# Optimization experiments

Measured on AMD Instinct MI355X. Metric: run time of the kernel, lower is better.

## Reference

```python
import jax, jax.numpy as jnp
import numpy as np

N_NODES = 100000
N_EDGES = 1600000
IN_C, HID, OUT_C = 128, 128, 64
LN_EPS = 1e-5


def _glorot(key, shape):
    fan_in = shape[-1]
    return jax.random.normal(key, shape, dtype=jnp.float32) / jnp.sqrt(jnp.float32(fan_in))


def setup_inputs() -> dict:
    key = jax.random.key(0)
    ks = jax.random.split(key, 16)
    x = jax.random.normal(ks[0], (N_NODES, IN_C), dtype=jnp.float32)
    edge_index = jax.random.randint(ks[1], (2, N_EDGES), 0, N_NODES, dtype=jnp.int64)
    inp = {"x": x, "edge_index": edge_index}
    dims = [(IN_C, HID), (HID, HID), (HID, OUT_C)]
    for i, (din, dout) in enumerate(dims):
        inp[f"Wl{i}"] = _glorot(ks[2 + 3 * i], (dout, din))   # neighbor-aggregate weight
        inp[f"Wr{i}"] = _glorot(ks[3 + 3 * i], (dout, din))   # root/self weight
        inp[f"b{i}"] = jnp.zeros((dout,), dtype=jnp.float32)
    for i, d in enumerate([HID, HID]):
        inp[f"g{i}"] = jnp.ones((d,), dtype=jnp.float32)      # LayerNorm gamma
        inp[f"be{i}"] = jnp.zeros((d,), dtype=jnp.float32)    # LayerNorm beta
    return inp


def sage_conv(x, src, dst, Wl, Wr, b):
    # mean aggregation of source features at destination nodes
    msg = x[src]                                                    # [E, F]
    agg = jax.ops.segment_sum(msg, dst, num_segments=N_NODES)      # [N, F]
    deg = jax.ops.segment_sum(jnp.ones((src.shape[0],), x.dtype), dst, num_segments=N_NODES)
    agg = agg / jnp.maximum(deg, 1.0)[:, None]
    return agg @ Wl.T + x @ Wr.T + b


def layer_norm(x, gamma, beta):
    mu = jnp.mean(x, axis=-1, keepdims=True)
    var = jnp.mean(jnp.square(x - mu), axis=-1, keepdims=True)
    return (x - mu) * jax.lax.rsqrt(var + LN_EPS) * gamma + beta


def reference(x, edge_index, Wl0, Wr0, b0, g0, be0, Wl1, Wr1, b1, g1, be1, Wl2, Wr2, b2):
    src, dst = edge_index[0], edge_index[1]
    h = layer_norm(jax.nn.relu(sage_conv(x, src, dst, Wl0, Wr0, b0)), g0, be0)
    h = layer_norm(jax.nn.relu(sage_conv(h, src, dst, Wl1, Wr1, b1)), g1, be1)
    return sage_conv(h, src, dst, Wl2, Wr2, b2)
```

## Files before the change

### kernel.cpp

```cpp
#include <hip/hip_runtime.h>


typedef __bf16 bf16x8 __attribute__((ext_vector_type(8)));
typedef __bf16 bf16x4 __attribute__((ext_vector_type(4)));
typedef float  f32x4  __attribute__((ext_vector_type(4)));

#define PB_SHIFT 9
#define PB_NB    256
#define PB_EPT   8
#define PB_BLOCK 256
#define PB_CHUNK (PB_BLOCK * PB_EPT)

__global__ __launch_bounds__(PB_BLOCK) void coarse_hist(
    const int* __restrict__ dst, int* __restrict__ bhist, int E) {
    __shared__ int h[PB_NB];
    const int t = threadIdx.x;
    h[t] = 0;
    __syncthreads();
    const int e0 = blockIdx.x * PB_CHUNK + t;
#pragma unroll
    for (int i = 0; i < PB_EPT; ++i) {
        int e = e0 + i * PB_BLOCK;
        if (e < E) atomicAdd(&h[dst[e] >> PB_SHIFT], 1);
    }
    __syncthreads();
    if (h[t]) atomicAdd(&bhist[t], h[t]);
}

__global__ __launch_bounds__(PB_NB) void coarse_scan(
    const int* __restrict__ bhist, int* __restrict__ bbase, int* __restrict__ bcur) {
    __shared__ int sm[PB_NB];
    const int t = threadIdx.x;
    int v = bhist[t];
    sm[t] = v;
    __syncthreads();
    for (int off = 1; off < PB_NB; off <<= 1) {
        int add = (t >= off) ? sm[t - off] : 0;
        __syncthreads();
        sm[t] += add;
        __syncthreads();
    }
    int excl = sm[t] - v;
    bbase[t] = excl;
    bcur[t] = excl;
}

__global__ __launch_bounds__(PB_BLOCK) void part_scatter(
    const int* __restrict__ src, const int* __restrict__ dst,
    int* __restrict__ bcursor, int2* __restrict__ part, int E) {
    __shared__ int hist[PB_NB];
    __shared__ int base[PB_NB];
    const int t = threadIdx.x;
    hist[t] = 0;
    __syncthreads();
    const int e0 = blockIdx.x * PB_CHUNK + t;
    int my_s[PB_EPT], my_d[PB_EPT], my_r[PB_EPT];
#pragma unroll
    for (int i = 0; i < PB_EPT; ++i) {
        int e = e0 + i * PB_BLOCK;
        if (e < E) {
            my_s[i] = src[e];
            my_d[i] = dst[e];
            my_r[i] = atomicAdd(&hist[my_d[i] >> PB_SHIFT], 1);
        }
    }
    __syncthreads();
    {
        int c = hist[t];
        base[t] = c ? atomicAdd(&bcursor[t], c) : 0;
    }
    __syncthreads();
#pragma unroll
    for (int i = 0; i < PB_EPT; ++i) {
        int e = e0 + i * PB_BLOCK;
        if (e < E) {
            int b = my_d[i] >> PB_SHIFT;
            part[base[b] + my_r[i]] = make_int2(my_s[i], my_d[i]);
        }
    }
}

__global__ __launch_bounds__(256) void bucket_build(
    const int2* __restrict__ part, const int* __restrict__ bbase,
    int* __restrict__ offs, int* __restrict__ ssrc, int N, int E) {
    __shared__ int h[512];
    __shared__ int s[512];
    __shared__ int cur[512];
    const int b = blockIdx.x;
    const int t = threadIdx.x;
    const int beg = bbase[b];
    const int end = (b == PB_NB - 1) ? E : bbase[b + 1];

    h[t] = 0; h[t + 256] = 0;
    __syncthreads();
    for (int e = beg + t; e < end; e += 256)
        atomicAdd(&h[part[e].y & 511], 1);
    __syncthreads();
    s[t] = h[t]; s[t + 256] = h[t + 256];
    __syncthreads();
    for (int off = 1; off < 512; off <<= 1) {
        int a0 = (t >= off) ? s[t - off] : 0;
        int i1 = t + 256;
        int a1 = (i1 >= off) ? s[i1 - off] : 0;
        __syncthreads();
        s[t] += a0; s[i1] += a1;
        __syncthreads();
    }
#pragma unroll
    for (int k = 0; k < 2; ++k) {
        int i = t + k * 256;
        int excl = s[i] - h[i];
        cur[i] = excl;
        int node = (b << PB_SHIFT) + i;
        if (node < N) offs[node] = beg + excl;
    }
    if (b == 0 && t == 0) offs[N] = E;
    __syncthreads();
    for (int e = beg + t; e < end; e += 256) {
        int2 sd = part[e];
        int p = atomicAdd(&cur[sd.y & 511], 1);
        ssrc[beg + p] = sd.x;
    }
}

template <typename AT, typename ZT>
__global__ __launch_bounds__(256) void gemm_mfma(
    const AT* __restrict__ A,
    const float* __restrict__ Wl,
    const float* __restrict__ Wr,
    const float* __restrict__ bias,
    __bf16* __restrict__ ybuf,
    ZT*     __restrict__ zbuf,
    int M, int dout) {
    __shared__ __bf16 Asm[64 * 136];
    __shared__ __bf16 Bsm[64 * 136];

    const int t = threadIdx.x;
    const int rowBase = blockIdx.x * 64;
    const int by = blockIdx.y;
    const int nyHalf = dout >> 6;
    const bool isZ = by >= nyHalf;
    const float* W = isZ ? Wr : Wl;
    const int colLocal = (by - (isZ ? nyHalf : 0)) * 64;

    if constexpr (sizeof(AT) == 4) {
#pragma unroll
        for (int i = 0; i < 8; ++i) {
            int idx = t + 256 * i;
            int r = idx >> 5;
            int c4 = idx & 31;
            int grow = rowBase + r;
            if (grow >= M) grow = M - 1;
            float4 v = *(const float4*)((const float*)A + (size_t)grow * 128 + c4 * 4);
            bf16x4 o;
            o[0] = (__bf16)v.x; o[1] = (__bf16)v.y; o[2] = (__bf16)v.z; o[3] = (__bf16)v.w;
            *(bf16x4*)(Asm + r * 136 + c4 * 4) = o;
        }
    } else {
#pragma unroll
        for (int i = 0; i < 4; ++i) {
            int idx = t + 256 * i;
            int r = idx >> 4;
            int c8 = idx & 15;
            int grow = rowBase + r;
            if (grow >= M) grow = M - 1;
            bf16x8 v = *(const bf16x8*)((const __bf16*)A + (size_t)grow * 128 + c8 * 8);
            *(bf16x8*)(Asm + r * 136 + c8 * 8) = v;
        }
    }
#pragma unroll
    for (int i = 0; i < 8; ++i) {
        int idx = t + 256 * i;
        int r = idx >> 5;
        int c4 = idx & 31;
        float4 v = *(const float4*)(W + (size_t)(colLocal + r) * 128 + c4 * 4);
        bf16x4 o;
        o[0] = (__bf16)v.x; o[1] = (__bf16)v.y; o[2] = (__bf16)v.z; o[3] = (__bf16)v.w;
        *(bf16x4*)(Bsm + r * 136 + c4 * 4) = o;
    }
    __syncthreads();

    const int lane = t & 63;
    const int wid = t >> 6;
    const int mb = (wid >> 1) * 32;
    const int nb = (wid & 1) * 32;
    const int ln = lane & 15;
    const int qk = lane >> 4;

    f32x4 acc[2][2] = {};
#pragma unroll
    for (int ks = 0; ks < 4; ++ks) {
        const int k0 = ks * 32 + qk * 8;
        bf16x8 a0 = *(const bf16x8*)(Asm + (mb + ln) * 136 + k0);
        bf16x8 a1 = *(const bf16x8*)(Asm + (mb + 16 + ln) * 136 + k0);
        bf16x8 b0 = *(const bf16x8*)(Bsm + (nb + ln) * 136 + k0);
        bf16x8 b1 = *(const bf16x8*)(Bsm + (nb + 16 + ln) * 136 + k0);
        acc[0][0] = __builtin_amdgcn_mfma_f32_16x16x32_bf16(a0, b0, acc[0][0], 0, 0, 0);
        acc[0][1] = __builtin_amdgcn_mfma_f32_16x16x32_bf16(a0, b1, acc[0][1], 0, 0, 0);
        acc[1][0] = __builtin_amdgcn_mfma_f32_16x16x32_bf16(a1, b0, acc[1][0], 0, 0, 0);
        acc[1][1] = __builtin_amdgcn_mfma_f32_16x16x32_bf16(a1, b1, acc[1][1], 0, 0, 0);
    }

#pragma unroll
    for (int i = 0; i < 2; ++i) {
#pragma unroll
        for (int r = 0; r < 4; ++r) {
            int grow = rowBase + mb + i * 16 + qk * 4 + r;
            if (grow >= M) continue;
#pragma unroll
            for (int j = 0; j < 2; ++j) {
                int col = colLocal + nb + j * 16 + ln;
                float v = acc[i][j][r];
                if (isZ) zbuf[(size_t)grow * dout + col] = (ZT)(v + bias[col]);
                else     ybuf[(size_t)grow * dout + col] = (__bf16)v;
            }
        }
    }
}

__global__ __launch_bounds__(256) void agg_ln128(
    const int* __restrict__ offs, const int* __restrict__ ssrc,
    const __bf16* __restrict__ ybuf,
    const __bf16* __restrict__ zbuf,
    const float* __restrict__ gamma, const float* __restrict__ beta,
    __bf16* __restrict__ hout, int nNodes) {
    const int lane = threadIdx.x & 63;
    const int qh = lane >> 4;
    const int li = lane & 15;
    const int node = blockIdx.x * 4 + (threadIdx.x >> 6);
    if (node >= nNodes) return;
    const int beg = offs[node], end = offs[node + 1];

    float acc[8] = {};
    for (int j = beg; j < end; j += 64) {
        int cnt = end - j;
        if (cnt > 64) cnt = 64;
        int sidx = ssrc[j + ((lane < cnt) ? lane : 0)];
        int quads = (cnt + 3) >> 2;
        for (int u = 0; u < quads; ++u) {
            int e = 4 * u + qh;
            int s = __shfl(sidx, (e < cnt) ? e : 0, 64);
            if (e < cnt) {
                bf16x8 v = *(const bf16x8*)(ybuf + (size_t)s * 128 + li * 8);
#pragma unroll
                for (int m = 0; m < 8; ++m) acc[m] += (float)v[m];
            }
        }
    }
#pragma unroll
    for (int m = 0; m < 8; ++m) {
        acc[m] += __shfl_xor(acc[m], 16, 64);
        acc[m] += __shfl_xor(acc[m], 32, 64);
    }
    int degn = end - beg;
    float inv = 1.f / (float)((degn > 1) ? degn : 1);
    bf16x8 zv = *(const bf16x8*)(zbuf + (size_t)node * 128 + li * 8);
    float v[8];
#pragma unroll
    for (int m = 0; m < 8; ++m) v[m] = fmaxf(acc[m] * inv + (float)zv[m], 0.f);

    float s = 0.f;
#pragma unroll
    for (int m = 0; m < 8; ++m) s += v[m];
#pragma unroll
    for (int off = 8; off >= 1; off >>= 1) s += __shfl_xor(s, off, 64);
    float mu = s * (1.f / 128.f);
    float d[8], q = 0.f;
#pragma unroll
    for (int m = 0; m < 8; ++m) { d[m] = v[m] - mu; q += d[m] * d[m]; }
#pragma unroll
    for (int off = 8; off >= 1; off >>= 1) q += __shfl_xor(q, off, 64);
    float rstd = rsqrtf(q * (1.f / 128.f) + 1e-5f);

    if (qh == 0) {
        const float4* g4 = (const float4*)(gamma + li * 8);
        const float4* b4 = (const float4*)(beta + li * 8);
        float4 g0 = g4[0], g1 = g4[1], bb0 = b4[0], bb1 = b4[1];
        bf16x8 o;
        o[0] = (__bf16)(d[0] * rstd * g0.x + bb0.x);
        o[1] = (__bf16)(d[1] * rstd * g0.y + bb0.y);
        o[2] = (__bf16)(d[2] * rstd * g0.z + bb0.z);
        o[3] = (__bf16)(d[3] * rstd * g0.w + bb0.w);
        o[4] = (__bf16)(d[4] * rstd * g1.x + bb1.x);
        o[5] = (__bf16)(d[5] * rstd * g1.y + bb1.y);
        o[6] = (__bf16)(d[6] * rstd * g1.z + bb1.z);
        o[7] = (__bf16)(d[7] * rstd * g1.w + bb1.w);
        *(bf16x8*)(hout + (size_t)node * 128 + li * 8) = o;
    }
}

__global__ __launch_bounds__(256) void agg_out64(
    const int* __restrict__ offs, const int* __restrict__ ssrc,
    const __bf16* __restrict__ ybuf,
    const float* __restrict__ zbuf,
    float* __restrict__ out, int nNodes) {
    const int lane = threadIdx.x & 63;
    const int eh = lane >> 3;
    const int li = lane & 7;
    const int node = blockIdx.x * 4 + (threadIdx.x >> 6);
    if (node >= nNodes) return;
    const int beg = offs[node], end = offs[node + 1];

    float acc[8] = {};
    for (int j = beg; j < end; j += 64) {
        int cnt = end - j;
        if (cnt > 64) cnt = 64;
        int sidx = ssrc[j + ((lane < cnt) ? lane : 0)];
        int octs = (cnt + 7) >> 3;
        for (int u = 0; u < octs; ++u) {
            int e = 8 * u + eh;
            int s = __shfl(sidx, (e < cnt) ? e : 0, 64);
            if (e < cnt) {
                bf16x8 v = *(const bf16x8*)(ybuf + (size_t)s * 64 + li * 8);
#pragma unroll
                for (int m = 0; m < 8; ++m) acc[m] += (float)v[m];
            }
        }
    }
#pragma unroll
    for (int m = 0; m < 8; ++m) {
        acc[m] += __shfl_xor(acc[m], 8, 64);
        acc[m] += __shfl_xor(acc[m], 16, 64);
        acc[m] += __shfl_xor(acc[m], 32, 64);
    }
    if (eh == 0) {
        int degn = end - beg;
        float inv = 1.f / (float)((degn > 1) ? degn : 1);
        const float4* z4 = (const float4*)(zbuf + (size_t)node * 64 + li * 8);
        float4 z0 = z4[0], z1 = z4[1];
        float4 o0, o1;
        o0.x = acc[0] * inv + z0.x;
        o0.y = acc[1] * inv + z0.y;
        o0.z = acc[2] * inv + z0.z;
        o0.w = acc[3] * inv + z0.w;
        o1.x = acc[4] * inv + z1.x;
        o1.y = acc[5] * inv + z1.y;
        o1.z = acc[6] * inv + z1.z;
        o1.w = acc[7] * inv + z1.w;
        float4* op = (float4*)(out + (size_t)node * 64 + li * 8);
        op[0] = o0;
        op[1] = o1;
    }
}

extern "C" void kernel_launch(void* const* d_in, const int* in_sizes, int n_in,
                              void* d_out, int out_size, void* d_ws, size_t ws_size,
                              hipStream_t stream) {
    const float* x   = (const float*)d_in[0];
    const int*   ei  = (const int*)d_in[1];
    const float* Wl0 = (const float*)d_in[2];
    const float* Wr0 = (const float*)d_in[3];
    const float* b0  = (const float*)d_in[4];
    const float* Wl1 = (const float*)d_in[5];
    const float* Wr1 = (const float*)d_in[6];
    const float* b1  = (const float*)d_in[7];
    const float* Wl2 = (const float*)d_in[8];
    const float* Wr2 = (const float*)d_in[9];
    const float* b2  = (const float*)d_in[10];
    const float* g0  = (const float*)d_in[11];
    const float* be0 = (const float*)d_in[12];
    const float* g1  = (const float*)d_in[13];
    const float* be1 = (const float*)d_in[14];

    const int N = in_sizes[0] / 128;
    const int E = in_sizes[1] / 2;
    const int* src = ei;
    const int* dst = ei + E;
    float* out = (float*)d_out;

    char* p = (char*)d_ws;
    auto carve = [&](size_t bytes) {
        void* q = (void*)p;
        p += (bytes + 255) & ~(size_t)255;
        return q;
    };
    int*     offs  = (int*)carve(sizeof(int) * (size_t)(N + 1));
    int*     bhist = (int*)carve(sizeof(int) * (size_t)PB_NB);
    int*     bbase = (int*)carve(sizeof(int) * (size_t)PB_NB);
    int*     bcur  = (int*)carve(sizeof(int) * (size_t)PB_NB);
    int*     ssrc  = (int*)carve(sizeof(int) * (size_t)E);
    int2*    part  = (int2*)carve(sizeof(int2) * (size_t)E);
    __bf16*  h     = (__bf16*)carve(sizeof(__bf16) * (size_t)N * 128);
    __bf16*  ybuf  = (__bf16*)carve(sizeof(__bf16) * (size_t)N * 128);
    void*    zraw  = carve(sizeof(__bf16) * (size_t)N * 128);
    __bf16*  zb    = (__bf16*)zraw;
    float*   zf    = (float*)zraw;

    hipMemsetAsync(bhist, 0, sizeof(int) * PB_NB, stream);
    const int gridE = (E + PB_CHUNK - 1) / PB_CHUNK;
    coarse_hist<<<gridE, PB_BLOCK, 0, stream>>>(dst, bhist, E);
    coarse_scan<<<1, PB_NB, 0, stream>>>(bhist, bbase, bcur);
    part_scatter<<<gridE, PB_BLOCK, 0, stream>>>(src, dst, bcur, part, E);
    bucket_build<<<PB_NB, 256, 0, stream>>>(part, bbase, offs, ssrc, N, E);

    const int gridM = (N + 63) / 64;
    const int gridNode = (N + 3) / 4;

    gemm_mfma<float, __bf16><<<dim3(gridM, 4), 256, 0, stream>>>(x, Wl0, Wr0, b0, ybuf, zb, N, 128);
    agg_ln128<<<gridNode, 256, 0, stream>>>(offs, ssrc, ybuf, zb, g0, be0, h, N);
    gemm_mfma<__bf16, __bf16><<<dim3(gridM, 4), 256, 0, stream>>>(h, Wl1, Wr1, b1, ybuf, zb, N, 128);
    agg_ln128<<<gridNode, 256, 0, stream>>>(offs, ssrc, ybuf, zb, g1, be1, h, N);
    gemm_mfma<__bf16, float><<<dim3(gridM, 2), 256, 0, stream>>>(h, Wl2, Wr2, b2, ybuf, zf, N, 64);
    agg_out64<<<gridNode, 256, 0, stream>>>(offs, ssrc, ybuf, zf, out, N);
}
```

Baseline: 455.4 us.

## Widen GEMM tiles to full output width and prefetch neighbor indices in aggregation

The GEMM kernel is templated on output width so each block computes all output columns for its row tile. This halves the grid and avoids loading and converting the A tile twice per weight. The aggregation kernels replace the chunked shuffle-based index broadcast with direct per-lane index loads, prefetched one iteration ahead, and use bit-shift bf16-to-float conversion. The trade-off is more LDS and accumulator registers per GEMM block and more scalar index loads per lane.

```diff
diff --git a/kernel.cpp b/kernel.cpp
--- a/kernel.cpp
+++ b/kernel.cpp
@@ -123,7 +123,7 @@
     }
 }
 
-template <typename AT, typename ZT>
+template <int DOUT, typename AT, typename ZT>
 __global__ __launch_bounds__(256) void gemm_mfma(
     const AT* __restrict__ A,
     const float* __restrict__ Wl,
@@ -131,17 +131,14 @@
     const float* __restrict__ bias,
     __bf16* __restrict__ ybuf,
     ZT*     __restrict__ zbuf,
-    int M, int dout) {
+    int M) {
     __shared__ __bf16 Asm[64 * 136];
-    __shared__ __bf16 Bsm[64 * 136];
+    __shared__ __bf16 Bsm[DOUT * 136];
 
     const int t = threadIdx.x;
     const int rowBase = blockIdx.x * 64;
-    const int by = blockIdx.y;
-    const int nyHalf = dout >> 6;
-    const bool isZ = by >= nyHalf;
+    const bool isZ = blockIdx.y != 0;
     const float* W = isZ ? Wr : Wl;
-    const int colLocal = (by - (isZ ? nyHalf : 0)) * 64;
 
     if constexpr (sizeof(AT) == 4) {
 #pragma unroll
@@ -168,12 +165,13 @@
             *(bf16x8*)(Asm + r * 136 + c8 * 8) = v;
         }
     }
-#pragma unroll
-    for (int i = 0; i < 8; ++i) {
+    constexpr int BCH = DOUT * 32 / 256;
+#pragma unroll
+    for (int i = 0; i < BCH; ++i) {
         int idx = t + 256 * i;
         int r = idx >> 5;
         int c4 = idx & 31;
-        float4 v = *(const float4*)(W + (size_t)(colLocal + r) * 128 + c4 * 4);
+        float4 v = *(const float4*)(W + (size_t)r * 128 + c4 * 4);
         bf16x4 o;
         o[0] = (__bf16)v.x; o[1] = (__bf16)v.y; o[2] = (__bf16)v.z; o[3] = (__bf16)v.w;
         *(bf16x4*)(Bsm + r * 136 + c4 * 4) = o;
@@ -183,24 +181,33 @@
     const int lane = t & 63;
     const int wid = t >> 6;
     const int mb = (wid >> 1) * 32;
-    const int nb = (wid & 1) * 32;
+    const int nbase = (wid & 1) * (DOUT / 2);
+    constexpr int NJ = DOUT / 32;
     const int ln = lane & 15;
     const int qk = lane >> 4;
 
-    f32x4 acc[2][2] = {};
+    f32x4 acc[2][NJ] = {};
 #pragma unroll
     for (int ks = 0; ks < 4; ++ks) {
         const int k0 = ks * 32 + qk * 8;
         bf16x8 a0 = *(const bf16x8*)(Asm + (mb + ln) * 136 + k0);
         bf16x8 a1 = *(const bf16x8*)(Asm + (mb + 16 + ln) * 136 + k0);
-        bf16x8 b0 = *(const bf16x8*)(Bsm + (nb + ln) * 136 + k0);
-        bf16x8 b1 = *(const bf16x8*)(Bsm + (nb + 16 + ln) * 136 + k0);
-        acc[0][0] = __builtin_amdgcn_mfma_f32_16x16x32_bf16(a0, b0, acc[0][0], 0, 0, 0);
-        acc[0][1] = __builtin_amdgcn_mfma_f32_16x16x32_bf16(a0, b1, acc[0][1], 0, 0, 0);
-        acc[1][0] = __builtin_amdgcn_mfma_f32_16x16x32_bf16(a1, b0, acc[1][0], 0, 0, 0);
-        acc[1][1] = __builtin_amdgcn_mfma_f32_16x16x32_bf16(a1, b1, acc[1][1], 0, 0, 0);
-    }
-
+        bf16x8 b[NJ];
+#pragma unroll
+        for (int j = 0; j < NJ; ++j)
+            b[j] = *(const bf16x8*)(Bsm + (nbase + j * 16 + ln) * 136 + k0);
+#pragma unroll
+        for (int j = 0; j < NJ; ++j) {
+            acc[0][j] = __builtin_amdgcn_mfma_f32_16x16x32_bf16(a0, b[j], acc[0][j], 0, 0, 0);
+            acc[1][j] = __builtin_amdgcn_mfma_f32_16x16x32_bf16(a1, b[j], acc[1][j], 0, 0, 0);
+        }
+    }
+
+    float bcol[NJ];
+    if (isZ) {
+#pragma unroll
+        for (int j = 0; j < NJ; ++j) bcol[j] = bias[nbase + j * 16 + ln];
+    }
 #pragma unroll
     for (int i = 0; i < 2; ++i) {
 #pragma unroll
@@ -208,11 +215,11 @@
             int grow = rowBase + mb + i * 16 + qk * 4 + r;
             if (grow >= M) continue;
 #pragma unroll
-            for (int j = 0; j < 2; ++j) {
-                int col = colLocal + nb + j * 16 + ln;
+            for (int j = 0; j < NJ; ++j) {
+                int col = nbase + j * 16 + ln;
                 float v = acc[i][j][r];
-                if (isZ) zbuf[(size_t)grow * dout + col] = (ZT)(v + bias[col]);
-                else     ybuf[(size_t)grow * dout + col] = (__bf16)v;
+                if (isZ) zbuf[(size_t)grow * DOUT + col] = (ZT)(v + bcol[j]);
+                else     ybuf[(size_t)grow * DOUT + col] = (__bf16)v;
             }
         }
     }
@@ -230,30 +237,35 @@
     const int node = blockIdx.x * 4 + (threadIdx.x >> 6);
     if (node >= nNodes) return;
     const int beg = offs[node], end = offs[node + 1];
+    const int deg = end - beg;
 
     float acc[8] = {};
-    for (int j = beg; j < end; j += 64) {
-        int cnt = end - j;
-        if (cnt > 64) cnt = 64;
-        int sidx = ssrc[j + ((lane < cnt) ? lane : 0)];
-        int quads = (cnt + 3) >> 2;
-        for (int u = 0; u < quads; ++u) {
-            int e = 4 * u + qh;
-            int s = __shfl(sidx, (e < cnt) ? e : 0, 64);
-            if (e < cnt) {
-                bf16x8 v = *(const bf16x8*)(ybuf + (size_t)s * 128 + li * 8);
-#pragma unroll
-                for (int m = 0; m < 8; ++m) acc[m] += (float)v[m];
-            }
-        }
+    const int iters = (deg + 3) >> 2;
+    int e = beg + qh;
+    int idx = 0;
+    if (iters > 0) idx = ssrc[(e < end) ? e : beg];
+    for (int u = 0; u < iters; ++u) {
+        int en = e + 4;
+        int idxN = ssrc[(en < end) ? en : beg];
+        if (e < end) {
+            uint4 uv = *(const uint4*)(ybuf + (size_t)idx * 128 + li * 8);
+            acc[0] += __uint_as_float(uv.x << 16);
+            acc[1] += __uint_as_float(uv.x & 0xffff0000u);
+            acc[2] += __uint_as_float(uv.y << 16);
+            acc[3] += __uint_as_float(uv.y & 0xffff0000u);
+            acc[4] += __uint_as_float(uv.z << 16);
+            acc[5] += __uint_as_float(uv.z & 0xffff0000u);
+            acc[6] += __uint_as_float(uv.w << 16);
+            acc[7] += __uint_as_float(uv.w & 0xffff0000u);
+        }
+        e = en; idx = idxN;
     }
 #pragma unroll
     for (int m = 0; m < 8; ++m) {
         acc[m] += __shfl_xor(acc[m], 16, 64);
         acc[m] += __shfl_xor(acc[m], 32, 64);
     }
-    int degn = end - beg;
-    float inv = 1.f / (float)((degn > 1) ? degn : 1);
+    float inv = 1.f / (float)((deg > 1) ? deg : 1);
     bf16x8 zv = *(const bf16x8*)(zbuf + (size_t)node * 128 + li * 8);
     float v[8];
 #pragma unroll
@@ -300,22 +312,28 @@
     const int node = blockIdx.x * 4 + (threadIdx.x >> 6);
     if (node >= nNodes) return;
     const int beg = offs[node], end = offs[node + 1];
+    const int deg = end - beg;
 
     float acc[8] = {};
-    for (int j = beg; j < end; j += 64) {
-        int cnt = end - j;
-        if (cnt > 64) cnt = 64;
-        int sidx = ssrc[j + ((lane < cnt) ? lane : 0)];
-        int octs = (cnt + 7) >> 3;
-        for (int u = 0; u < octs; ++u) {
-            int e = 8 * u + eh;
-            int s = __shfl(sidx, (e < cnt) ? e : 0, 64);
-            if (e < cnt) {
-                bf16x8 v = *(const bf16x8*)(ybuf + (size_t)s * 64 + li * 8);
-#pragma unroll
-                for (int m = 0; m < 8; ++m) acc[m] += (float)v[m];
-            }
-        }
+    const int iters = (deg + 7) >> 3;
+    int e = beg + eh;
+    int idx = 0;
+    if (iters > 0) idx = ssrc[(e < end) ? e : beg];
+    for (int u = 0; u < iters; ++u) {
+        int en = e + 8;
+        int idxN = ssrc[(en < end) ? en : beg];
+        if (e < end) {
+            uint4 uv = *(const uint4*)(ybuf + (size_t)idx * 64 + li * 8);
+            acc[0] += __uint_as_float(uv.x << 16);
+            acc[1] += __uint_as_float(uv.x & 0xffff0000u);
+            acc[2] += __uint_as_float(uv.y << 16);
+            acc[3] += __uint_as_float(uv.y & 0xffff0000u);
+            acc[4] += __uint_as_float(uv.z << 16);
+            acc[5] += __uint_as_float(uv.z & 0xffff0000u);
+            acc[6] += __uint_as_float(uv.w << 16);
+            acc[7] += __uint_as_float(uv.w & 0xffff0000u);
+        }
+        e = en; idx = idxN;
     }
 #pragma unroll
     for (int m = 0; m < 8; ++m) {
@@ -324,8 +342,7 @@
         acc[m] += __shfl_xor(acc[m], 32, 64);
     }
     if (eh == 0) {
-        int degn = end - beg;
-        float inv = 1.f / (float)((degn > 1) ? degn : 1);
+        float inv = 1.f / (float)((deg > 1) ? deg : 1);
         const float4* z4 = (const float4*)(zbuf + (size_t)node * 64 + li * 8);
         float4 z0 = z4[0], z1 = z4[1];
         float4 o0, o1;
@@ -396,10 +413,10 @@
     const int gridM = (N + 63) / 64;
     const int gridNode = (N + 3) / 4;
 
-    gemm_mfma<float, __bf16><<<dim3(gridM, 4), 256, 0, stream>>>(x, Wl0, Wr0, b0, ybuf, zb, N, 128);
+    gemm_mfma<128, float, __bf16><<<dim3(gridM, 2), 256, 0, stream>>>(x, Wl0, Wr0, b0, ybuf, zb, N);
     agg_ln128<<<gridNode, 256, 0, stream>>>(offs, ssrc, ybuf, zb, g0, be0, h, N);
-    gemm_mfma<__bf16, __bf16><<<dim3(gridM, 4), 256, 0, stream>>>(h, Wl1, Wr1, b1, ybuf, zb, N, 128);
+    gemm_mfma<128, __bf16, __bf16><<<dim3(gridM, 2), 256, 0, stream>>>(h, Wl1, Wr1, b1, ybuf, zb, N);
     agg_ln128<<<gridNode, 256, 0, stream>>>(offs, ssrc, ybuf, zb, g1, be1, h, N);
-    gemm_mfma<__bf16, float><<<dim3(gridM, 2), 256, 0, stream>>>(h, Wl2, Wr2, b2, ybuf, zf, N, 64);
+    gemm_mfma<64, __bf16, float><<<dim3(gridM, 2), 256, 0, stream>>>(h, Wl2, Wr2, b2, ybuf, zf, N);
     agg_out64<<<gridNode, 256, 0, stream>>>(offs, ssrc, ybuf, zf, out, N);
 }
```

New measurement: 425.0 us. 6.7% less time.
